# Performance work log

Measured on AMD Instinct MI355X. Metric: run time of the kernel, lower is better.

## Reference

```python
import jax, jax.numpy as jnp
import numpy as np

N_NODES = 50000


def setup_inputs() -> dict:
    key = jax.random.key(0)
    k1, k2, k3, k4, k5, k6 = jax.random.split(key, 6)
    N, E, D, F = 50000, 800000, 512, 256
    feature_ori = jax.random.normal(k1, (N, D), dtype=jnp.float32)
    feature_aug = jax.random.normal(k2, (N, D), dtype=jnp.float32)
    edge_row = jax.random.randint(k3, (E,), 0, N, dtype=jnp.int32)
    edge_col = jax.random.randint(k4, (E,), 0, N, dtype=jnp.int32)
    edge_val = jax.random.uniform(k5, (E,), dtype=jnp.float32)
    # kaiming-uniform-ish init for weight, zeros for bias (as in reset_parameters)
    bound = float(np.sqrt(6.0 / D))
    weight = jax.random.uniform(k6, (D, F), dtype=jnp.float32, minval=-bound, maxval=bound)
    bias = jnp.zeros((F,), dtype=jnp.float32)
    return {
        "feature_ori": feature_ori,
        "feature_aug": feature_aug,
        "edge_row": edge_row,
        "edge_col": edge_col,
        "edge_val": edge_val,
        "weight": weight,
        "bias": bias,
    }


def _branch(feat, weight, bias, edge_row, edge_col, edge_val):
    # support = X @ W  -> [N, F]
    support = feat @ weight
    # sparse aggregation: out[i] = sum_{e: row[e]=i} val[e] * support[col[e]]
    msgs = edge_val[:, None] * support[edge_col]          # [E, F]
    out = jax.ops.segment_sum(msgs, edge_row, num_segments=N_NODES)
    return jax.nn.relu(out + bias)


def reference(feature_ori, feature_aug, edge_row, edge_col, edge_val, weight, bias):
    out_ori = _branch(feature_ori, weight, bias, edge_row, edge_col, edge_val)
    out_aug = _branch(feature_aug, weight, bias, edge_row, edge_col, edge_val)
    return (out_ori, out_aug)
```

## Files before the change

### kernel.cpp

```cpp
#include <hip/hip_runtime.h>
#include <hip/hip_bf16.h>

#define NNODES 50000
#define NEDGES 800000
#define DIN    512
#define FOUT   256

typedef __attribute__((ext_vector_type(8))) short short8;
typedef __attribute__((ext_vector_type(4))) float f32x4;
typedef __attribute__((ext_vector_type(4))) unsigned int u32x4;
typedef __attribute__((ext_vector_type(4))) unsigned short usv4;
typedef __attribute__((ext_vector_type(8))) unsigned short usv8;

static __device__ __forceinline__ unsigned short f2bf(float f) {
    unsigned int u = __float_as_uint(f);
    u += 0x7FFF + ((u >> 16) & 1);
    return (unsigned short)(u >> 16);
}
static __device__ __forceinline__ float bf2f(unsigned short h) {
    return __uint_as_float(((unsigned int)h) << 16);
}

__global__ void prep_kernel(const float* __restrict__ W, unsigned short* __restrict__ Wt,
                            const int* __restrict__ row, int* __restrict__ cnt) {
    int b = blockIdx.x;
    if (b < 512) {
        int o = b * 256 + threadIdx.x;
        int n = o >> 9, k = o & 511;
        Wt[o] = f2bf(W[k * FOUT + n]);
    } else {
        int e = (b - 512) * 256 + threadIdx.x;
        if (e < NEDGES) atomicAdd(&cnt[row[e]], 1);
    }
}

__global__ void scan_partial(const int* __restrict__ cnt, int* __restrict__ partial) {
    __shared__ int sm[256];
    int i = blockIdx.x * 256 + threadIdx.x;
    int v = (i < NNODES) ? cnt[i] : 0;
    sm[threadIdx.x] = v; __syncthreads();
    for (int s = 128; s > 0; s >>= 1) {
        if (threadIdx.x < s) sm[threadIdx.x] += sm[threadIdx.x + s];
        __syncthreads();
    }
    if (threadIdx.x == 0) partial[blockIdx.x] = sm[0];
}

__global__ void scan_exclusive_small(int* __restrict__ partial, int nb) {
    __shared__ int sm[256];
    int t = threadIdx.x;
    int v = (t < nb) ? partial[t] : 0;
    sm[t] = v; __syncthreads();
    for (int off = 1; off < 256; off <<= 1) {
        int add = (t >= off) ? sm[t - off] : 0;
        __syncthreads();
        sm[t] += add;
        __syncthreads();
    }
    if (t < nb) partial[t] = sm[t] - v;
}

__global__ void scan_write(const int* __restrict__ cnt, const int* __restrict__ partial,
                           int* __restrict__ row_start, int* __restrict__ cursor) {
    __shared__ int sm[256];
    int t = threadIdx.x;
    int i = blockIdx.x * 256 + t;
    int v = (i < NNODES) ? cnt[i] : 0;
    sm[t] = v; __syncthreads();
    for (int off = 1; off < 256; off <<= 1) {
        int add = (t >= off) ? sm[t - off] : 0;
        __syncthreads();
        sm[t] += add;
        __syncthreads();
    }
    if (i < NNODES) {
        int rs = partial[blockIdx.x] + sm[t] - v;
        row_start[i] = rs;
        cursor[i] = rs;
    }
    if (i == 0) row_start[NNODES] = NEDGES;
}

__global__ void scatter_kernel(const int* __restrict__ row, const int* __restrict__ col,
                               const float* __restrict__ val,
                               int* __restrict__ cursor, unsigned int* __restrict__ cv) {
    int e = blockIdx.x * 256 + threadIdx.x;
    if (e < NEDGES) {
        int r = row[e];
        int pos = atomicAdd(&cursor[r], 1);
        unsigned int vb = f2bf(val[e]);
        cv[pos] = (vb << 16) | (unsigned int)col[e];
    }
}

__global__ __launch_bounds__(512, 2)
void gemm_kernel(const float* __restrict__ Xo, const float* __restrict__ Xa,
                 const unsigned short* __restrict__ Wt,
                 unsigned short* __restrict__ S) {
    __shared__ __align__(16) unsigned short As[2][128][40];
    __shared__ __align__(16) unsigned short Bs[2][256][40];
    const int tid = threadIdx.x;
    const int branch = blockIdx.z;
    const float* __restrict__ X = branch ? Xa : Xo;
    const int boff = branch * 256;
    const int m_base = blockIdx.x * 128;
    const int lane = tid & 63, wave = tid >> 6;
    const int wm = (wave >> 2) * 64, wn = (wave & 3) * 64;
    const int quad = lane >> 4, r16 = lane & 15;

    f32x4 acc[4][4] = {};

    const int arow = tid >> 2;
    const int acol = (tid & 3) * 8;
    const int kseg = (tid & 3) * 8;
    const int nrow = tid >> 2;

    const int gm = m_base + arow;
    const bool va = gm < NNODES;
    const float* pA = &X[(long)gm * DIN + acol];
    const unsigned short* pB0 = &Wt[(long)nrow * DIN + kseg];
    const unsigned short* pB1 = &Wt[(long)(128 + nrow) * DIN + kseg];

    f32x4 fa0A, fa1A, fa0B, fa1B;
    u32x4 ub0A, ub1A, ub0B, ub1B;

#define GEMM_LOAD(SET, K0)                                                     \
    do {                                                                       \
        fa0##SET = va ? __builtin_nontemporal_load((const f32x4*)(pA + (K0)))  \
                      : (f32x4)0.f;                                            \
        fa1##SET = va ? __builtin_nontemporal_load((const f32x4*)(pA + (K0) + 4))\
                      : (f32x4)0.f;                                            \
        ub0##SET = *(const u32x4*)(pB0 + (K0));                                \
        ub1##SET = *(const u32x4*)(pB1 + (K0));                                \
    } while (0)

#define GEMM_WRITE(SET, B)                                                     \
    do {                                                                       \
        usv8 h;                                                                \
        h[0] = f2bf(fa0##SET[0]); h[1] = f2bf(fa0##SET[1]);                    \
        h[2] = f2bf(fa0##SET[2]); h[3] = f2bf(fa0##SET[3]);                    \
        h[4] = f2bf(fa1##SET[0]); h[5] = f2bf(fa1##SET[1]);                    \
        h[6] = f2bf(fa1##SET[2]); h[7] = f2bf(fa1##SET[3]);                    \
        *(usv8*)&As[B][arow][acol] = h;                                        \
        *(u32x4*)&Bs[B][nrow][kseg] = ub0##SET;                                \
        *(u32x4*)&Bs[B][128 + nrow][kseg] = ub1##SET;                          \
    } while (0)

#define GEMM_COMPUTE(B)                                                        \
    do {                                                                       \
        short8 a_frag[4], b_frag[4];                                           \
        _Pragma("unroll")                                                      \
        for (int mi = 0; mi < 4; mi++)                                         \
            a_frag[mi] = *(const short8*)&As[B][wm + mi * 16 + r16][quad * 8]; \
        _Pragma("unroll")                                                      \
        for (int ni = 0; ni < 4; ni++)                                         \
            b_frag[ni] = *(const short8*)&Bs[B][wn + ni * 16 + r16][quad * 8]; \
        _Pragma("unroll")                                                      \
        for (int mi = 0; mi < 4; mi++)                                         \
            _Pragma("unroll")                                                  \
            for (int ni = 0; ni < 4; ni++)                                     \
                acc[mi][ni] = __builtin_amdgcn_mfma_f32_16x16x32_bf16(         \
                    a_frag[mi], b_frag[ni], acc[mi][ni], 0, 0, 0);             \
    } while (0)

#define GEMM_BARRIER()                                                         \
    do {                                                                       \
        asm volatile("s_waitcnt lgkmcnt(0)" ::: "memory");                     \
        __builtin_amdgcn_s_barrier();                                          \
        __builtin_amdgcn_sched_barrier(0);                                     \
    } while (0)

    GEMM_LOAD(A, 0);
    GEMM_WRITE(A, 0);
    GEMM_LOAD(A, 32);
    GEMM_BARRIER();

    #pragma unroll
    for (int t = 0; t < 16; t += 2) {
        if (t + 2 < 16) GEMM_LOAD(B, (t + 2) * 32);
        GEMM_COMPUTE(0);
        GEMM_WRITE(A, 1);
        GEMM_BARRIER();
        if (t + 3 < 16) GEMM_LOAD(A, (t + 3) * 32);
        GEMM_COMPUTE(1);
        if (t + 2 < 16) {
            GEMM_WRITE(B, 0);
            GEMM_BARRIER();
        }
    }

#undef GEMM_LOAD
#undef GEMM_WRITE
#undef GEMM_COMPUTE
#undef GEMM_BARRIER

    #pragma unroll
    for (int mi = 0; mi < 4; mi++) {
        #pragma unroll
        for (int rr = 0; rr < 4; rr++) {
            int m = m_base + wm + mi * 16 + quad * 4 + rr;
            if (m < NNODES) {
                #pragma unroll
                for (int ni = 0; ni < 4; ni++) {
                    int n = wn + ni * 16 + r16;
                    S[(long)m * 512 + boff + n] = f2bf(acc[mi][ni][rr]);
                }
            }
        }
    }
}

__global__ __launch_bounds__(256)
void aggregate_pass(const int* __restrict__ row_start,
                    const unsigned int* __restrict__ cv,
                    const unsigned short* __restrict__ S,
                    const float* __restrict__ bias, float* __restrict__ out,
                    const int half) {
    const int node = __builtin_amdgcn_readfirstlane(blockIdx.x * 4 + (threadIdx.x >> 6));
    if (node >= NNODES) return;
    const int lane = threadIdx.x & 63;
    const int fl = (lane & 31) * 8;
    const unsigned int sub = lane >> 5;
    const long soff = (long)half * 256 + fl;
    const int s = row_start[node], e = row_start[node + 1];

    float a0 = 0.f, a1 = 0.f, a2 = 0.f, a3 = 0.f;
    float a4 = 0.f, a5 = 0.f, a6 = 0.f, a7 = 0.f;

#define PLOAD(CW0, CW1, Q)                                                     \
    do {                                                                       \
        unsigned int cw_ = sub ? (CW1) : (CW0);                                \
        Q = *(const usv8*)&S[(long)(cw_ & 0xFFFFu) * 512 + soff];              \
    } while (0)

#define PFMA(CW0, CW1, Q)                                                      \
    do {                                                                       \
        unsigned int cw_ = sub ? (CW1) : (CW0);                                \
        float v = bf2f((unsigned short)(cw_ >> 16));                           \
        a0 = fmaf(v, bf2f((Q)[0]), a0); a1 = fmaf(v, bf2f((Q)[1]), a1);        \
        a2 = fmaf(v, bf2f((Q)[2]), a2); a3 = fmaf(v, bf2f((Q)[3]), a3);        \
        a4 = fmaf(v, bf2f((Q)[4]), a4); a5 = fmaf(v, bf2f((Q)[5]), a5);        \
        a6 = fmaf(v, bf2f((Q)[6]), a6); a7 = fmaf(v, bf2f((Q)[7]), a7);        \
    } while (0)

#define LOADG(C0, C1, C2, C3, C4, C5, C6, C7, Q0, Q1, Q2, Q3, I)               \
    do {                                                                       \
        C0 = cv[(I)];     C1 = cv[(I) + 1]; C2 = cv[(I) + 2]; C3 = cv[(I) + 3];\
        C4 = cv[(I) + 4]; C5 = cv[(I) + 5]; C6 = cv[(I) + 6]; C7 = cv[(I) + 7];\
        PLOAD(C0, C1, Q0); PLOAD(C2, C3, Q1);                                  \
        PLOAD(C4, C5, Q2); PLOAD(C6, C7, Q3);                                  \
    } while (0)

#define FMAG(C0, C1, C2, C3, C4, C5, C6, C7, Q0, Q1, Q2, Q3)                   \
    do {                                                                       \
        PFMA(C0, C1, Q0); PFMA(C2, C3, Q1);                                    \
        PFMA(C4, C5, Q2); PFMA(C6, C7, Q3);                                    \
    } while (0)

    unsigned int c0, c1, c2, c3, c4, c5, c6, c7;
    unsigned int d0, d1, d2, d3, d4, d5, d6, d7;
    usv8 qa0, qa1, qa2, qa3, qb0, qb1, qb2, qb3;

    int idx = s;
    int r = (e - s) >> 3;
    if (r > 0) {
        LOADG(c0, c1, c2, c3, c4, c5, c6, c7, qa0, qa1, qa2, qa3, idx); idx += 8; r--;
        while (r >= 2) {
            LOADG(d0, d1, d2, d3, d4, d5, d6, d7, qb0, qb1, qb2, qb3, idx); idx += 8;
            FMAG(c0, c1, c2, c3, c4, c5, c6, c7, qa0, qa1, qa2, qa3);
            LOADG(c0, c1, c2, c3, c4, c5, c6, c7, qa0, qa1, qa2, qa3, idx); idx += 8;
            FMAG(d0, d1, d2, d3, d4, d5, d6, d7, qb0, qb1, qb2, qb3);
            r -= 2;
        }
        if (r == 1) {
            LOADG(d0, d1, d2, d3, d4, d5, d6, d7, qb0, qb1, qb2, qb3, idx); idx += 8;
            FMAG(c0, c1, c2, c3, c4, c5, c6, c7, qa0, qa1, qa2, qa3);
            FMAG(d0, d1, d2, d3, d4, d5, d6, d7, qb0, qb1, qb2, qb3);
        } else {
            FMAG(c0, c1, c2, c3, c4, c5, c6, c7, qa0, qa1, qa2, qa3);
        }
    }
    for (; idx + 2 <= e; idx += 2) {
        unsigned int w0 = cv[idx], w1 = cv[idx + 1];
        usv8 q;
        PLOAD(w0, w1, q);
        PFMA(w0, w1, q);
    }
    if (idx < e) {
        unsigned int w = cv[idx];
        usv8 q = *(const usv8*)&S[(long)(w & 0xFFFFu) * 512 + soff];
        float v = sub ? 0.f : bf2f((unsigned short)(w >> 16));
        a0 = fmaf(v, bf2f(q[0]), a0); a1 = fmaf(v, bf2f(q[1]), a1);
        a2 = fmaf(v, bf2f(q[2]), a2); a3 = fmaf(v, bf2f(q[3]), a3);
        a4 = fmaf(v, bf2f(q[4]), a4); a5 = fmaf(v, bf2f(q[5]), a5);
        a6 = fmaf(v, bf2f(q[6]), a6); a7 = fmaf(v, bf2f(q[7]), a7);
    }

#undef PLOAD
#undef PFMA
#undef LOADG
#undef FMAG

    a0 += __shfl_xor(a0, 32); a1 += __shfl_xor(a1, 32);
    a2 += __shfl_xor(a2, 32); a3 += __shfl_xor(a3, 32);
    a4 += __shfl_xor(a4, 32); a5 += __shfl_xor(a5, 32);
    a6 += __shfl_xor(a6, 32); a7 += __shfl_xor(a7, 32);

    if (lane < 32) {
        f32x4 b0 = *(const f32x4*)&bias[fl];
        f32x4 b1 = *(const f32x4*)&bias[fl + 4];
        long o = (long)half * NNODES * FOUT + (long)node * FOUT + fl;
        f32x4 r0, r1;
        r0[0] = fmaxf(a0 + b0[0], 0.f); r0[1] = fmaxf(a1 + b0[1], 0.f);
        r0[2] = fmaxf(a2 + b0[2], 0.f); r0[3] = fmaxf(a3 + b0[3], 0.f);
        r1[0] = fmaxf(a4 + b1[0], 0.f); r1[1] = fmaxf(a5 + b1[1], 0.f);
        r1[2] = fmaxf(a6 + b1[2], 0.f); r1[3] = fmaxf(a7 + b1[3], 0.f);
        __builtin_nontemporal_store(r0, (f32x4*)&out[o]);
        __builtin_nontemporal_store(r1, (f32x4*)&out[o + 4]);
    }
}

extern "C" void kernel_launch(void* const* d_in, const int* in_sizes, int n_in,
                              void* d_out, int out_size, void* d_ws, size_t ws_size,
                              hipStream_t stream) {
    const float* Xo   = (const float*)d_in[0];
    const float* Xa   = (const float*)d_in[1];
    const int*   erow = (const int*)d_in[2];
    const int*   ecol = (const int*)d_in[3];
    const float* eval_= (const float*)d_in[4];
    const float* W    = (const float*)d_in[5];
    const float* bias = (const float*)d_in[6];
    float* out = (float*)d_out;

    char* ws = (char*)d_ws;
    unsigned short* S         = (unsigned short*)(ws);
    unsigned short* Wt        = (unsigned short*)(ws + 51200000);
    int*            cnt       = (int*)(ws + 51462144);
    int*            row_start = (int*)(ws + 51662144);
    int*            partial   = (int*)(ws + 51862208);
    unsigned int*   cv        = (unsigned int*)(ws + 51863232);

    (void)in_sizes; (void)n_in; (void)out_size; (void)ws_size;

    hipMemsetAsync(cnt, 0, 200000, stream);
    prep_kernel<<<3637, 256, 0, stream>>>(W, Wt, erow, cnt);
    scan_partial<<<196, 256, 0, stream>>>(cnt, partial);
    scan_exclusive_small<<<1, 256, 0, stream>>>(partial, 196);
    scan_write<<<196, 256, 0, stream>>>(cnt, partial, row_start, cnt);
    scatter_kernel<<<3125, 256, 0, stream>>>(erow, ecol, eval_, cnt, cv);

    dim3 gg(391, 1, 2);
    gemm_kernel<<<gg, 512, 0, stream>>>(Xo, Xa, Wt, S);

    aggregate_pass<<<12500, 256, 0, stream>>>(row_start, cv, S, bias, out, 0);
    aggregate_pass<<<12500, 256, 0, stream>>>(row_start, cv, S, bias, out, 1);
}
```

Before: 469.1 us.

## Shrink GEMM tile to 64x256 with 256-thread blocks and single-buffered register prefetch

The GEMM block tile drops from 128x256 with 8 waves to 64x256 with 4 waves, doubling the grid to 782x2 blocks, and each thread now loads four B rows. The pipeline is simplified to one register staging set with a single-iteration loop that writes the next LDS buffer before computing the current one. The aim is better occupancy and load balance across CUs and lower register pressure. In exchange, each block reads the full W tile for half as many rows, which doubles B traffic per output row, and the prefetch depth is shallower.

```diff
diff --git a/kernel.cpp b/kernel.cpp
--- a/kernel.cpp
+++ b/kernel.cpp
@@ -93,57 +93,61 @@
     }
 }
 
-__global__ __launch_bounds__(512, 2)
+__global__ __launch_bounds__(256, 3)
 void gemm_kernel(const float* __restrict__ Xo, const float* __restrict__ Xa,
                  const unsigned short* __restrict__ Wt,
                  unsigned short* __restrict__ S) {
-    __shared__ __align__(16) unsigned short As[2][128][40];
+    __shared__ __align__(16) unsigned short As[2][64][40];
     __shared__ __align__(16) unsigned short Bs[2][256][40];
     const int tid = threadIdx.x;
     const int branch = blockIdx.z;
     const float* __restrict__ X = branch ? Xa : Xo;
     const int boff = branch * 256;
-    const int m_base = blockIdx.x * 128;
+    const int m_base = blockIdx.x * 64;
     const int lane = tid & 63, wave = tid >> 6;
-    const int wm = (wave >> 2) * 64, wn = (wave & 3) * 64;
+    const int wn = wave * 64;
     const int quad = lane >> 4, r16 = lane & 15;
 
     f32x4 acc[4][4] = {};
 
     const int arow = tid >> 2;
     const int acol = (tid & 3) * 8;
-    const int kseg = (tid & 3) * 8;
-    const int nrow = tid >> 2;
 
     const int gm = m_base + arow;
     const bool va = gm < NNODES;
     const float* pA = &X[(long)gm * DIN + acol];
-    const unsigned short* pB0 = &Wt[(long)nrow * DIN + kseg];
-    const unsigned short* pB1 = &Wt[(long)(128 + nrow) * DIN + kseg];
-
-    f32x4 fa0A, fa1A, fa0B, fa1B;
-    u32x4 ub0A, ub1A, ub0B, ub1B;
-
-#define GEMM_LOAD(SET, K0)                                                     \
-    do {                                                                       \
-        fa0##SET = va ? __builtin_nontemporal_load((const f32x4*)(pA + (K0)))  \
-                      : (f32x4)0.f;                                            \
-        fa1##SET = va ? __builtin_nontemporal_load((const f32x4*)(pA + (K0) + 4))\
-                      : (f32x4)0.f;                                            \
-        ub0##SET = *(const u32x4*)(pB0 + (K0));                                \
-        ub1##SET = *(const u32x4*)(pB1 + (K0));                                \
-    } while (0)
-
-#define GEMM_WRITE(SET, B)                                                     \
+    const unsigned short* pB0 = &Wt[(long)(arow) * DIN + acol];
+    const unsigned short* pB1 = &Wt[(long)(64 + arow) * DIN + acol];
+    const unsigned short* pB2 = &Wt[(long)(128 + arow) * DIN + acol];
+    const unsigned short* pB3 = &Wt[(long)(192 + arow) * DIN + acol];
+
+    f32x4 fa0, fa1;
+    u32x4 ub0, ub1, ub2, ub3;
+
+#define GEMM_LOAD(K0)                                                          \
+    do {                                                                       \
+        fa0 = va ? __builtin_nontemporal_load((const f32x4*)(pA + (K0)))       \
+                 : (f32x4)0.f;                                                 \
+        fa1 = va ? __builtin_nontemporal_load((const f32x4*)(pA + (K0) + 4))   \
+                 : (f32x4)0.f;                                                 \
+        ub0 = *(const u32x4*)(pB0 + (K0));                                     \
+        ub1 = *(const u32x4*)(pB1 + (K0));                                     \
+        ub2 = *(const u32x4*)(pB2 + (K0));                                     \
+        ub3 = *(const u32x4*)(pB3 + (K0));                                     \
+    } while (0)
+
+#define GEMM_WRITE(B)                                                          \
     do {                                                                       \
         usv8 h;                                                                \
-        h[0] = f2bf(fa0##SET[0]); h[1] = f2bf(fa0##SET[1]);                    \
-        h[2] = f2bf(fa0##SET[2]); h[3] = f2bf(fa0##SET[3]);                    \
-        h[4] = f2bf(fa1##SET[0]); h[5] = f2bf(fa1##SET[1]);                    \
-        h[6] = f2bf(fa1##SET[2]); h[7] = f2bf(fa1##SET[3]);                    \
+        h[0] = f2bf(fa0[0]); h[1] = f2bf(fa0[1]);                              \
+        h[2] = f2bf(fa0[2]); h[3] = f2bf(fa0[3]);                              \
+        h[4] = f2bf(fa1[0]); h[5] = f2bf(fa1[1]);                              \
+        h[6] = f2bf(fa1[2]); h[7] = f2bf(fa1[3]);                              \
         *(usv8*)&As[B][arow][acol] = h;                                        \
-        *(u32x4*)&Bs[B][nrow][kseg] = ub0##SET;                                \
-        *(u32x4*)&Bs[B][128 + nrow][kseg] = ub1##SET;                          \
+        *(u32x4*)&Bs[B][arow][acol] = ub0;                                     \
+        *(u32x4*)&Bs[B][64 + arow][acol] = ub1;                                \
+        *(u32x4*)&Bs[B][128 + arow][acol] = ub2;                               \
+        *(u32x4*)&Bs[B][192 + arow][acol] = ub3;                               \
     } while (0)
 
 #define GEMM_COMPUTE(B)                                                        \
@@ -151,7 +155,7 @@
         short8 a_frag[4], b_frag[4];                                           \
         _Pragma("unroll")                                                      \
         for (int mi = 0; mi < 4; mi++)                                         \
-            a_frag[mi] = *(const short8*)&As[B][wm + mi * 16 + r16][quad * 8]; \
+            a_frag[mi] = *(const short8*)&As[B][mi * 16 + r16][quad * 8];      \
         _Pragma("unroll")                                                      \
         for (int ni = 0; ni < 4; ni++)                                         \
             b_frag[ni] = *(const short8*)&Bs[B][wn + ni * 16 + r16][quad * 8]; \
@@ -170,23 +174,17 @@
         __builtin_amdgcn_sched_barrier(0);                                     \
     } while (0)
 
-    GEMM_LOAD(A, 0);
-    GEMM_WRITE(A, 0);
-    GEMM_LOAD(A, 32);
+    GEMM_LOAD(0);
+    GEMM_WRITE(0);
+    GEMM_LOAD(32);
     GEMM_BARRIER();
 
     #pragma unroll
-    for (int t = 0; t < 16; t += 2) {
-        if (t + 2 < 16) GEMM_LOAD(B, (t + 2) * 32);
-        GEMM_COMPUTE(0);
-        GEMM_WRITE(A, 1);
-        GEMM_BARRIER();
-        if (t + 3 < 16) GEMM_LOAD(A, (t + 3) * 32);
-        GEMM_COMPUTE(1);
-        if (t + 2 < 16) {
-            GEMM_WRITE(B, 0);
-            GEMM_BARRIER();
-        }
+    for (int t = 0; t < 16; ++t) {
+        if (t < 15) GEMM_WRITE((t + 1) & 1);
+        if (t + 2 < 16) GEMM_LOAD((t + 2) * 32);
+        GEMM_COMPUTE(t & 1);
+        if (t < 15) GEMM_BARRIER();
     }
 
 #undef GEMM_LOAD
@@ -198,7 +196,7 @@
     for (int mi = 0; mi < 4; mi++) {
         #pragma unroll
         for (int rr = 0; rr < 4; rr++) {
-            int m = m_base + wm + mi * 16 + quad * 4 + rr;
+            int m = m_base + mi * 16 + quad * 4 + rr;
             if (m < NNODES) {
                 #pragma unroll
                 for (int ni = 0; ni < 4; ni++) {
@@ -349,8 +347,8 @@
     scan_write<<<196, 256, 0, stream>>>(cnt, partial, row_start, cnt);
     scatter_kernel<<<3125, 256, 0, stream>>>(erow, ecol, eval_, cnt, cv);
 
-    dim3 gg(391, 1, 2);
-    gemm_kernel<<<gg, 512, 0, stream>>>(Xo, Xa, Wt, S);
+    dim3 gg(782, 1, 2);
+    gemm_kernel<<<gg, 256, 0, stream>>>(Xo, Xa, Wt, S);
 
     aggregate_pass<<<12500, 256, 0, stream>>>(row_start, cv, S, bias, out, 0);
     aggregate_pass<<<12500, 256, 0, stream>>>(row_start, cv, S, bias, out, 1);
```

After: 484.8 us. +3.3%, slower.

## Load GEMM weight tiles directly into LDS and re-pipeline the k-loop

Applied to the files above, without the earlier changes.

The B (weight) tiles of the bf16 GEMM are now fetched with global_load_lds, which writes global memory straight into LDS instead of going through registers and explicit LDS stores. The Bs layout loses its padding (row stride 40 to 32) because the direct-to-LDS path needs contiguous destinations. The k-loop is restructured into a single-step double-buffered pipeline with explicit vmcnt waits around the async copies. The aim is to cut register pressure and VALU/LDS-store work for the B operand. The unpadded layout risks LDS bank conflicts on the b-fragment reads, and the GEMM is likely a minor share of the total time.

```diff
diff --git a/kernel.cpp b/kernel.cpp
--- a/kernel.cpp
+++ b/kernel.cpp
@@ -19,6 +19,12 @@
 }
 static __device__ __forceinline__ float bf2f(unsigned short h) {
     return __uint_as_float(((unsigned int)h) << 16);
+}
+
+static __device__ __forceinline__ void gload_lds16(const void* g, void* l) {
+    __builtin_amdgcn_global_load_lds(
+        (const __attribute__((address_space(1))) unsigned int*)g,
+        (__attribute__((address_space(3))) unsigned int*)l, 16, 0, 0);
 }
 
 __global__ void prep_kernel(const float* __restrict__ W, unsigned short* __restrict__ Wt,
@@ -98,7 +104,7 @@
                  const unsigned short* __restrict__ Wt,
                  unsigned short* __restrict__ S) {
     __shared__ __align__(16) unsigned short As[2][128][40];
-    __shared__ __align__(16) unsigned short Bs[2][256][40];
+    __shared__ __align__(16) unsigned short Bs[2][256][32];
     const int tid = threadIdx.x;
     const int branch = blockIdx.z;
     const float* __restrict__ X = branch ? Xa : Xo;
@@ -112,29 +118,32 @@
 
     const int arow = tid >> 2;
     const int acol = (tid & 3) * 8;
-    const int kseg = (tid & 3) * 8;
-    const int nrow = tid >> 2;
-
     const int gm = m_base + arow;
     const bool va = gm < NNODES;
     const float* pA = &X[(long)gm * DIN + acol];
-    const unsigned short* pB0 = &Wt[(long)nrow * DIN + kseg];
-    const unsigned short* pB1 = &Wt[(long)(128 + nrow) * DIN + kseg];
+
+    const int brow0 = wave * 32 + (lane >> 2);
+    const unsigned short* pB0 = &Wt[(long)brow0 * DIN + (lane & 3) * 8];
+    const unsigned short* pB1 = &Wt[(long)(brow0 + 16) * DIN + (lane & 3) * 8];
 
     f32x4 fa0A, fa1A, fa0B, fa1B;
-    u32x4 ub0A, ub1A, ub0B, ub1B;
-
-#define GEMM_LOAD(SET, K0)                                                     \
+
+#define GEMM_GLOADB(T, B)                                                      \
+    do {                                                                       \
+        const int k0_ = (T) * 32;                                              \
+        gload_lds16(pB0 + k0_, &Bs[B][wave * 32][0]);                          \
+        gload_lds16(pB1 + k0_, &Bs[B][wave * 32 + 16][0]);                     \
+    } while (0)
+
+#define GEMM_LOADA(SET, K0)                                                    \
     do {                                                                       \
         fa0##SET = va ? __builtin_nontemporal_load((const f32x4*)(pA + (K0)))  \
                       : (f32x4)0.f;                                            \
         fa1##SET = va ? __builtin_nontemporal_load((const f32x4*)(pA + (K0) + 4))\
                       : (f32x4)0.f;                                            \
-        ub0##SET = *(const u32x4*)(pB0 + (K0));                                \
-        ub1##SET = *(const u32x4*)(pB1 + (K0));                                \
-    } while (0)
-
-#define GEMM_WRITE(SET, B)                                                     \
+    } while (0)
+
+#define GEMM_WRITEA(SET, B)                                                    \
     do {                                                                       \
         usv8 h;                                                                \
         h[0] = f2bf(fa0##SET[0]); h[1] = f2bf(fa0##SET[1]);                    \
@@ -142,8 +151,6 @@
         h[4] = f2bf(fa1##SET[0]); h[5] = f2bf(fa1##SET[1]);                    \
         h[6] = f2bf(fa1##SET[2]); h[7] = f2bf(fa1##SET[3]);                    \
         *(usv8*)&As[B][arow][acol] = h;                                        \
-        *(u32x4*)&Bs[B][nrow][kseg] = ub0##SET;                                \
-        *(u32x4*)&Bs[B][128 + nrow][kseg] = ub1##SET;                          \
     } while (0)
 
 #define GEMM_COMPUTE(B)                                                        \
@@ -163,36 +170,39 @@
                     a_frag[mi], b_frag[ni], acc[mi][ni], 0, 0, 0);             \
     } while (0)
 
-#define GEMM_BARRIER()                                                         \
-    do {                                                                       \
-        asm volatile("s_waitcnt lgkmcnt(0)" ::: "memory");                     \
-        __builtin_amdgcn_s_barrier();                                          \
-        __builtin_amdgcn_sched_barrier(0);                                     \
-    } while (0)
-
-    GEMM_LOAD(A, 0);
-    GEMM_WRITE(A, 0);
-    GEMM_LOAD(A, 32);
-    GEMM_BARRIER();
+    GEMM_LOADA(A, 0);
+    GEMM_GLOADB(0, 0);
+    GEMM_LOADA(B, 32);
+    GEMM_WRITEA(A, 0);
+    asm volatile("s_waitcnt vmcnt(2)" ::: "memory");
+    asm volatile("s_waitcnt lgkmcnt(0)" ::: "memory");
+    __builtin_amdgcn_s_barrier();
+    __builtin_amdgcn_sched_barrier(0);
 
     #pragma unroll
-    for (int t = 0; t < 16; t += 2) {
-        if (t + 2 < 16) GEMM_LOAD(B, (t + 2) * 32);
-        GEMM_COMPUTE(0);
-        GEMM_WRITE(A, 1);
-        GEMM_BARRIER();
-        if (t + 3 < 16) GEMM_LOAD(A, (t + 3) * 32);
-        GEMM_COMPUTE(1);
+    for (int t = 0; t < 16; ++t) {
+        if (t + 1 < 16) GEMM_GLOADB(t + 1, (t + 1) & 1);
+        __builtin_amdgcn_sched_barrier(0);
+        if (t + 1 < 16) {
+            if (((t + 1) & 1) == 0) GEMM_WRITEA(A, 0); else GEMM_WRITEA(B, 1);
+        }
         if (t + 2 < 16) {
-            GEMM_WRITE(B, 0);
-            GEMM_BARRIER();
-        }
-    }
-
-#undef GEMM_LOAD
-#undef GEMM_WRITE
+            if ((t & 1) == 0) GEMM_LOADA(A, (t + 2) * 32); else GEMM_LOADA(B, (t + 2) * 32);
+        }
+        GEMM_COMPUTE(t & 1);
+        if (t < 15) {
+            if (t <= 13) asm volatile("s_waitcnt vmcnt(2)" ::: "memory");
+            else         asm volatile("s_waitcnt vmcnt(0)" ::: "memory");
+            asm volatile("s_waitcnt lgkmcnt(0)" ::: "memory");
+            __builtin_amdgcn_s_barrier();
+            __builtin_amdgcn_sched_barrier(0);
+        }
+    }
+
+#undef GEMM_GLOADB
+#undef GEMM_LOADA
+#undef GEMM_WRITEA
 #undef GEMM_COMPUTE
-#undef GEMM_BARRIER
 
     #pragma unroll
     for (int mi = 0; mi < 4; mi++) {
```

Result: slower. 482.1 us (+2.8%).
